# Optimization experiments

Hardware: AMD Instinct MI355X
Metric: run time of the kernel (lower is better)

## Reference

```python
import jax, jax.numpy as jnp
import numpy as np

B, L, H, D = 16, 4096, 16, 64
HID = H * D


def setup_inputs() -> dict:
    key = jax.random.key(0)
    ks = jax.random.split(key, 10)
    w = lambda k: jax.random.normal(k, (HID, HID), jnp.float32) * 0.02
    return dict(
        hidden_states=jax.random.normal(ks[0], (B, 1, HID), jnp.float32),
        past_key=jax.random.normal(ks[1], (B, H, L, D), jnp.float32),
        past_value=jax.random.normal(ks[2], (B, H, L, D), jnp.float32),
        attention_mask=jnp.ones((B, L), jnp.float32),
        cache_position=jax.random.randint(ks[3], (B, 1), 0, L, jnp.int32),
        Wq=w(ks[4]), bq=jnp.zeros((HID,), jnp.float32),
        Wk=w(ks[5]), bk=jnp.zeros((HID,), jnp.float32),
        Wv=w(ks[6]), bv=jnp.zeros((HID,), jnp.float32),
        Wo=w(ks[7]), bo=jnp.zeros((HID,), jnp.float32),
    )


def reference(hidden_states, past_key, past_value, attention_mask, cache_position,
              Wq, bq, Wk, bk, Wv, bv, Wo, bo):
    # projections: [B,1,HID]; torch Linear => x @ W.T + b
    q = hidden_states @ Wq.T + bq
    k = hidden_states @ Wk.T + bk
    v = hidden_states @ Wv.T + bv
    # [B,H,1,D]
    q = q.reshape(B, 1, H, D).transpose(0, 2, 1, 3)
    k_new = k.reshape(B, H, D)
    v_new = v.reshape(B, H, D)
    pos = cache_position[:, 0]  # [B]
    bidx = jnp.arange(B)
    # write new token K/V into cache at cache_position (per-batch)
    k_cache = past_key.at[bidx, :, pos].set(k_new)
    v_cache = past_value.at[bidx, :, pos].set(v_new)
    scale = jnp.float32(1.0) / jnp.sqrt(jnp.float32(D))
    scores = jnp.einsum('bhqd,bhkd->bhqk', q, k_cache) * scale  # [B,H,1,L]
    neg = jnp.finfo(scores.dtype).min
    scores = jnp.where(attention_mask[:, None, None, :] > 0, scores, neg)
    p = jax.nn.softmax(scores, axis=-1)
    ctx = jnp.einsum('bhqk,bhkd->bhqd', p, v_cache)  # [B,H,1,D]
    attn_output = ctx.transpose(0, 2, 1, 3).reshape(B, 1, HID) @ Wo.T + bo
    return attn_output, k_cache, v_cache
```

## Files before the change

kernel.cpp:

```cpp
#include <hip/hip_runtime.h>
#include <hip/hip_bf16.h>

#define BATCH 16
#define SEQL  4096
#define NH    16
#define HD    64
#define HID   1024
#define NCHUNK 8
#define CHUNK  (SEQL / NCHUNK)
#define KV_ELEMS (BATCH * NH * SEQL * HD)
#define PSTRIDE 68
#define C2 0.1803368801f

typedef float f4 __attribute__((ext_vector_type(4)));

__global__ __launch_bounds__(256) void gemv3(
    const float* __restrict__ x,
    const float* __restrict__ W0, const float* __restrict__ W1,
    const float* __restrict__ W2,
    const float* __restrict__ b0, const float* __restrict__ b1,
    const float* __restrict__ b2,
    float* __restrict__ out)
{
    __shared__ float xs[BATCH * HID];
    const int t = threadIdx.x;
    {
        const f4* src = (const f4*)x;
        f4* dst = (f4*)xs;
        #pragma unroll
        for (int i = 0; i < (BATCH * HID / 4) / 256; ++i)
            dst[t + i * 256] = src[t + i * 256];
    }
    __syncthreads();

    const int which = blockIdx.x >> 8;
    const int ob    = (blockIdx.x & 255) << 2;
    const float* W    = (which == 0) ? W0 : ((which == 1) ? W1 : W2);
    const float* bias = (which == 0) ? b0 : ((which == 1) ? b1 : b2);
    const int col = t >> 6, lane = t & 63;
    const int o = ob + col;
    const float* wrow = W + (size_t)o * HID;

    float acc[BATCH];
    #pragma unroll
    for (int b = 0; b < BATCH; ++b) acc[b] = 0.f;

    #pragma unroll
    for (int i = 0; i < 4; ++i) {
        const int k = (lane << 2) + (i << 8);
        const f4 w4 = *(const f4*)&wrow[k];
        #pragma unroll
        for (int b = 0; b < BATCH; ++b) {
            const f4 h4 = *(const f4*)&xs[b * HID + k];
            acc[b] += w4.x * h4.x + w4.y * h4.y + w4.z * h4.z + w4.w * h4.w;
        }
    }

    #pragma unroll
    for (int b = 0; b < BATCH; ++b) {
        #pragma unroll
        for (int sh = 1; sh < 64; sh <<= 1)
            acc[b] += __shfl_xor(acc[b], sh);
    }
    if (lane == 0) {
        const float bb = bias[o];
        #pragma unroll
        for (int b = 0; b < BATCH; ++b)
            out[which * (BATCH * HID) + b * HID + o] = acc[b] + bb;
    }
}

__global__ __launch_bounds__(256, 6) void attn_fused(
    const float* __restrict__ qkv,
    const float* __restrict__ past_k,
    const float* __restrict__ past_v,
    const float* __restrict__ mask,
    float* __restrict__ kout,
    float* __restrict__ vout,
    float* __restrict__ part)
{
    const int bh = blockIdx.x;
    const int c  = blockIdx.y;
    const int b  = bh >> 4;
    const int h  = bh & 15;
    const int t  = threadIdx.x;
    const int g  = t >> 4;
    const int j  = t & 15;

    const f4 q4 = *(const f4*)&qkv[b * HID + h * HD + (j << 2)];

    const size_t base = (size_t)bh * (SEQL * HD);
    const float* __restrict__ pkb = past_k + base;
    const float* __restrict__ pvb = past_v + base;
    float* __restrict__ kob = kout + base;
    float* __restrict__ vob = vout + base;
    const float* __restrict__ mrow = mask + b * SEQL;

    float l = 0.f;
    f4 a4 = {0.f, 0.f, 0.f, 0.f};

    #pragma unroll 1
    for (int s = 0; s < CHUNK / 128; ++s) {
        const int r0 = c * CHUNK + s * 128 + g;
        const int o0 = r0 * HD + (j << 2);

        f4 kx[8];
        float am[8];
        #pragma unroll
        for (int u = 0; u < 8; ++u)
            kx[u] = __builtin_nontemporal_load((const f4*)(pkb + o0 + u * (16 * HD)));
        #pragma unroll
        for (int u = 0; u < 8; ++u)
            am[u] = mrow[r0 + u * 16];
        #pragma unroll
        for (int u = 0; u < 8; ++u)
            __builtin_nontemporal_store(kx[u], (f4*)(kob + o0 + u * (16 * HD)));

        float p[8];
        #pragma unroll
        for (int u = 0; u < 8; ++u) {
            float d = kx[u].x * q4.x + kx[u].y * q4.y
                    + kx[u].z * q4.z + kx[u].w * q4.w;
            d += __shfl_xor(d, 1);
            d += __shfl_xor(d, 2);
            d += __shfl_xor(d, 4);
            d += __shfl_xor(d, 8);
            float pe = exp2f(d * C2);
            p[u] = (am[u] > 0.f) ? pe : 0.f;
            l += p[u];
        }

        f4 vx[8];
        #pragma unroll
        for (int u = 0; u < 8; ++u)
            vx[u] = __builtin_nontemporal_load((const f4*)(pvb + o0 + u * (16 * HD)));
        #pragma unroll
        for (int u = 0; u < 8; ++u)
            __builtin_nontemporal_store(vx[u], (f4*)(vob + o0 + u * (16 * HD)));
        #pragma unroll
        for (int u = 0; u < 8; ++u) {
            a4.x += p[u] * vx[u].x;
            a4.y += p[u] * vx[u].y;
            a4.z += p[u] * vx[u].z;
            a4.w += p[u] * vx[u].w;
        }
    }

    __shared__ float sl_[16];
    __shared__ float sa[16][64];
    if (j == 0) sl_[g] = l;
    *(f4*)&sa[g][(j << 2)] = a4;
    __syncthreads();

    float* pr = part + ((size_t)bh * NCHUNK + c) * PSTRIDE;
    if (t < 64) {
        float A = 0.f;
        #pragma unroll
        for (int gg = 0; gg < 16; ++gg) A += sa[gg][t];
        pr[1 + t] = A;
    } else if (t == 64) {
        float L = 0.f;
        #pragma unroll
        for (int gg = 0; gg < 16; ++gg) L += sl_[gg];
        pr[0] = L;
    }
}

__global__ __launch_bounds__(64) void merge_fix(
    const float* __restrict__ qkv,
    const float* __restrict__ past_k,
    const float* __restrict__ past_v,
    const float* __restrict__ mask,
    const int*   __restrict__ cpos,
    float* __restrict__ kout,
    float* __restrict__ vout,
    const float* __restrict__ part,
    float* __restrict__ ctx)
{
    const int bh = blockIdx.x;
    const int b = bh >> 4, h = bh & 15;
    const int t = threadIdx.x;
    const int pos = cpos[b];

    const size_t rowoff = (size_t)bh * (SEQL * HD) + (size_t)pos * HD + t;
    const int qo = b * HID + h * HD + t;
    const float qd  = qkv[qo];
    const float knd = qkv[BATCH * HID + qo];
    const float vnd = qkv[2 * BATCH * HID + qo];
    const float ksd = past_k[rowoff];
    const float vsd = past_v[rowoff];

    kout[rowoff] = knd;
    vout[rowoff] = vnd;

    float dst = qd * ksd, dnw = qd * knd;
    #pragma unroll
    for (int sh = 1; sh < 64; sh <<= 1) {
        dst += __shfl_xor(dst, sh);
        dnw += __shfl_xor(dnw, sh);
    }
    const float am = mask[b * SEQL + pos];
    float ps = 0.f, pn = 0.f;
    if (am > 0.f) { ps = exp2f(dst * C2); pn = exp2f(dnw * C2); }

    const int cc0 = pos / CHUNK;
    float L = 0.f, A = 0.f;
    #pragma unroll
    for (int cc = 0; cc < NCHUNK; ++cc) {
        const float* pr = part + ((size_t)bh * NCHUNK + cc) * PSTRIDE;
        float Lc = pr[0];
        float Ac = pr[1 + t];
        if (cc == cc0) { Lc += pn - ps; Ac += pn * vnd - ps * vsd; }
        L += Lc;
        A += Ac;
    }
    ctx[bh * HD + t] = A / L;
}

extern "C" void kernel_launch(void* const* d_in, const int* in_sizes, int n_in,
                              void* d_out, int out_size, void* d_ws, size_t ws_size,
                              hipStream_t stream) {
    const float* hs   = (const float*)d_in[0];
    const float* pk   = (const float*)d_in[1];
    const float* pv   = (const float*)d_in[2];
    const float* mask = (const float*)d_in[3];
    const int*   cpos = (const int*)d_in[4];
    const float* Wq   = (const float*)d_in[5];
    const float* bq   = (const float*)d_in[6];
    const float* Wk   = (const float*)d_in[7];
    const float* bk   = (const float*)d_in[8];
    const float* Wv   = (const float*)d_in[9];
    const float* bv   = (const float*)d_in[10];
    const float* Wo   = (const float*)d_in[11];
    const float* bo   = (const float*)d_in[12];

    float* out_attn = (float*)d_out;
    float* kout = out_attn + BATCH * HID;
    float* vout = kout + KV_ELEMS;

    float* ws    = (float*)d_ws;
    float* qkv   = ws;
    float* ctx   = ws + 49152;
    float* apart = ws + 65536;

    gemv3<<<dim3(768), 256, 0, stream>>>(hs, Wq, Wk, Wv, bq, bk, bv, qkv);

    attn_fused<<<dim3(256, NCHUNK), 256, 0, stream>>>(qkv, pk, pv, mask,
                                                      kout, vout, apart);
    merge_fix<<<dim3(256), 64, 0, stream>>>(qkv, pk, pv, mask, cpos,
                                            kout, vout, apart, ctx);

    gemv3<<<dim3(256), 256, 0, stream>>>(ctx, Wo, Wo, Wo, bo, bo, bo, out_attn);
}
```

Measured before the change: 219.6 us.

## Split fused attention into separate K-score and V-accumulate kernels

Replaces the single fused attention kernel with two kernels: one copies K, computes the masked exponentiated scores and writes them to a workspace along with partial denominators, and a second copies V and accumulates the weighted sum using those stored scores. The intent is to decouple the K and V streams so each kernel has a simpler memory access pattern and lower register pressure. The K/V loads also switch from nontemporal to ordinary loads. In exchange it adds an extra launch and a round trip of scores through global memory, and it takes the split path only when the workspace is large enough.

```diff
diff --git a/kernel.cpp b/kernel.cpp
--- a/kernel.cpp
+++ b/kernel.cpp
@@ -70,6 +70,125 @@
     }
 }
 
+__global__ __launch_bounds__(256, 6) void kcopy_score(
+    const float* __restrict__ qkv,
+    const float* __restrict__ past_k,
+    const float* __restrict__ mask,
+    float* __restrict__ kout,
+    float* __restrict__ pws,
+    float* __restrict__ part)
+{
+    const int bh = blockIdx.x, c = blockIdx.y;
+    const int b = bh >> 4, h = bh & 15;
+    const int t = threadIdx.x;
+    const int g = t >> 4, j = t & 15;
+
+    const f4 q4 = *(const f4*)&qkv[b * HID + h * HD + (j << 2)];
+    const size_t base = (size_t)bh * (SEQL * HD);
+    const float* __restrict__ pkb = past_k + base;
+    float* __restrict__ kob = kout + base;
+    const float* __restrict__ mrow = mask + b * SEQL;
+    float* __restrict__ prow = pws + bh * SEQL;
+
+    float l = 0.f;
+
+    #pragma unroll 1
+    for (int s = 0; s < CHUNK / 128; ++s) {
+        const int r0 = c * CHUNK + s * 128 + g;
+        const int o0 = r0 * HD + (j << 2);
+
+        f4 kx[8];
+        float am[8];
+        #pragma unroll
+        for (int u = 0; u < 8; ++u)
+            kx[u] = *(const f4*)(pkb + o0 + u * (16 * HD));
+        #pragma unroll
+        for (int u = 0; u < 8; ++u)
+            am[u] = mrow[r0 + u * 16];
+        #pragma unroll
+        for (int u = 0; u < 8; ++u)
+            __builtin_nontemporal_store(kx[u], (f4*)(kob + o0 + u * (16 * HD)));
+
+        #pragma unroll
+        for (int u = 0; u < 8; ++u) {
+            float d = kx[u].x * q4.x + kx[u].y * q4.y
+                    + kx[u].z * q4.z + kx[u].w * q4.w;
+            d += __shfl_xor(d, 1);
+            d += __shfl_xor(d, 2);
+            d += __shfl_xor(d, 4);
+            d += __shfl_xor(d, 8);
+            float pe = exp2f(d * C2);
+            const float p = (am[u] > 0.f) ? pe : 0.f;
+            l += p;
+            if (j == 0) prow[r0 + u * 16] = p;
+        }
+    }
+
+    __shared__ float sl_[16];
+    if (j == 0) sl_[g] = l;
+    __syncthreads();
+    if (t == 0) {
+        float L = 0.f;
+        #pragma unroll
+        for (int gg = 0; gg < 16; ++gg) L += sl_[gg];
+        part[((size_t)bh * NCHUNK + c) * PSTRIDE] = L;
+    }
+}
+
+__global__ __launch_bounds__(256, 6) void vcopy_acc(
+    const float* __restrict__ past_v,
+    float* __restrict__ vout,
+    const float* __restrict__ pws,
+    float* __restrict__ part)
+{
+    const int bh = blockIdx.x, c = blockIdx.y;
+    const int t = threadIdx.x;
+    const int g = t >> 4, j = t & 15;
+
+    const size_t base = (size_t)bh * (SEQL * HD);
+    const float* __restrict__ pvb = past_v + base;
+    float* __restrict__ vob = vout + base;
+    const float* __restrict__ prow = pws + bh * SEQL;
+
+    f4 a4 = {0.f, 0.f, 0.f, 0.f};
+
+    #pragma unroll 1
+    for (int s = 0; s < CHUNK / 128; ++s) {
+        const int r0 = c * CHUNK + s * 128 + g;
+        const int o0 = r0 * HD + (j << 2);
+
+        f4 vx[8];
+        float p[8];
+        #pragma unroll
+        for (int u = 0; u < 8; ++u)
+            vx[u] = *(const f4*)(pvb + o0 + u * (16 * HD));
+        #pragma unroll
+        for (int u = 0; u < 8; ++u)
+            p[u] = prow[r0 + u * 16];
+        #pragma unroll
+        for (int u = 0; u < 8; ++u)
+            __builtin_nontemporal_store(vx[u], (f4*)(vob + o0 + u * (16 * HD)));
+        #pragma unroll
+        for (int u = 0; u < 8; ++u) {
+            a4.x += p[u] * vx[u].x;
+            a4.y += p[u] * vx[u].y;
+            a4.z += p[u] * vx[u].z;
+            a4.w += p[u] * vx[u].w;
+        }
+    }
+
+    __shared__ float sa[16][64];
+    *(f4*)&sa[g][(j << 2)] = a4;
+    __syncthreads();
+
+    if (t < 64) {
+        float A = 0.f;
+        #pragma unroll
+        for (int gg = 0; gg < 16; ++gg) A += sa[gg][t];
+        part[((size_t)bh * NCHUNK + c) * PSTRIDE + 1 + t] = A;
+    }
+}
+
 __global__ __launch_bounds__(256, 6) void attn_fused(
     const float* __restrict__ qkv,
     const float* __restrict__ past_k,
@@ -79,16 +198,12 @@
     float* __restrict__ vout,
     float* __restrict__ part)
 {
-    const int bh = blockIdx.x;
-    const int c  = blockIdx.y;
-    const int b  = bh >> 4;
-    const int h  = bh & 15;
-    const int t  = threadIdx.x;
-    const int g  = t >> 4;
-    const int j  = t & 15;
+    const int bh = blockIdx.x, c = blockIdx.y;
+    const int b = bh >> 4, h = bh & 15;
+    const int t = threadIdx.x;
+    const int g = t >> 4, j = t & 15;
 
     const f4 q4 = *(const f4*)&qkv[b * HID + h * HD + (j << 2)];
-
     const size_t base = (size_t)bh * (SEQL * HD);
     const float* __restrict__ pkb = past_k + base;
     const float* __restrict__ pvb = past_v + base;
@@ -242,11 +357,21 @@
     float* qkv   = ws;
     float* ctx   = ws + 49152;
     float* apart = ws + 65536;
+    float* pws   = ws + 204800;
+
+    const bool split_ok = ws_size >= (size_t)1253376 * sizeof(float);
 
     gemv3<<<dim3(768), 256, 0, stream>>>(hs, Wq, Wk, Wv, bq, bk, bv, qkv);
 
-    attn_fused<<<dim3(256, NCHUNK), 256, 0, stream>>>(qkv, pk, pv, mask,
-                                                      kout, vout, apart);
+    if (split_ok) {
+        kcopy_score<<<dim3(256, NCHUNK), 256, 0, stream>>>(qkv, pk, mask,
+                                                           kout, pws, apart);
+        vcopy_acc<<<dim3(256, NCHUNK), 256, 0, stream>>>(pv, vout, pws, apart);
+    } else {
+        attn_fused<<<dim3(256, NCHUNK), 256, 0, stream>>>(qkv, pk, pv, mask,
+                                                          kout, vout, apart);
+    }
+
     merge_fix<<<dim3(256), 64, 0, stream>>>(qkv, pk, pv, mask, cpos,
                                             kout, vout, apart, ctx);
 
```

After: 229.9 us. +4.7%, slower.

## Replace chunked attention with grid-strided tile sweep and per-tile partials

Applied to the files above, without the earlier changes.

Adds a new attention kernel that splits the KV cache into 65536 tiles of 16 rows and sweeps them with 2048 persistent blocks in a grid-stride loop. Each iteration prefetches the next tile's K/V while copying and reducing the current one, and writes per-tile partial sums to workspace. A new merge kernel then reduces the 256 partials per head. The aim is more parallelism and software prefetching to keep HBM busy, at the cost of two block barriers per tile, more partial-sum traffic, and a dependence on the workspace being large enough (otherwise the old path runs).

```diff
diff --git a/kernel.cpp b/kernel.cpp
--- a/kernel.cpp
+++ b/kernel.cpp
@@ -6,11 +6,16 @@
 #define NH    16
 #define HD    64
 #define HID   1024
+#define KV_ELEMS (BATCH * NH * SEQL * HD)
+#define C2 0.1803368801f
+
+#define NBLK  2048
+#define NTILE 65536
+#define TPB   (NTILE / NBLK)
+
 #define NCHUNK 8
-#define CHUNK  (SEQL / NCHUNK)
-#define KV_ELEMS (BATCH * NH * SEQL * HD)
+#define CHUNK  512
 #define PSTRIDE 68
-#define C2 0.1803368801f
 
 typedef float f4 __attribute__((ext_vector_type(4)));
 
@@ -68,6 +73,133 @@
         for (int b = 0; b < BATCH; ++b)
             out[which * (BATCH * HID) + b * HID + o] = acc[b] + bb;
     }
+}
+
+__global__ __launch_bounds__(256, 8) void attn_sweep(
+    const float* __restrict__ qkv,
+    const float* __restrict__ past_k,
+    const float* __restrict__ past_v,
+    const float* __restrict__ mask,
+    float* __restrict__ kout,
+    float* __restrict__ vout,
+    float* __restrict__ Aws,
+    float* __restrict__ Lws)
+{
+    const int blk = blockIdx.x;
+    const int t   = threadIdx.x;
+    const int g   = t >> 4;
+    const int j   = t & 15;
+    const int w   = t >> 6;
+
+    __shared__ float sw[4][64];
+    __shared__ float slw[4];
+
+    int tile = blk;
+    size_t off = (size_t)tile * 1024 + (t << 2);
+    f4 k0 = __builtin_nontemporal_load((const f4*)(past_k + off));
+    f4 v0 = __builtin_nontemporal_load((const f4*)(past_v + off));
+    f4 q0 = *(const f4*)&qkv[(tile >> 8) * HD + (j << 2)];
+    float am0 = mask[((tile >> 12) << 12) + ((tile & 255) << 4) + g];
+
+    #pragma unroll 1
+    for (int tau = 0; tau < TPB; ++tau) {
+        const size_t coff = off;
+        const int ctile = tile;
+        const f4 kc = k0, vc = v0, qc = q0;
+        const float amc = am0;
+
+        if (tau < TPB - 1) {
+            tile += NBLK;
+            off = (size_t)tile * 1024 + (t << 2);
+            k0 = __builtin_nontemporal_load((const f4*)(past_k + off));
+            v0 = __builtin_nontemporal_load((const f4*)(past_v + off));
+            q0 = *(const f4*)&qkv[(tile >> 8) * HD + (j << 2)];
+            am0 = mask[((tile >> 12) << 12) + ((tile & 255) << 4) + g];
+        }
+
+        __builtin_nontemporal_store(kc, (f4*)(kout + coff));
+        __builtin_nontemporal_store(vc, (f4*)(vout + coff));
+
+        float d = kc.x * qc.x + kc.y * qc.y + kc.z * qc.z + kc.w * qc.w;
+        d += __shfl_xor(d, 1);
+        d += __shfl_xor(d, 2);
+        d += __shfl_xor(d, 4);
+        d += __shfl_xor(d, 8);
+        float pe = exp2f(d * C2);
+        const float p = (amc > 0.f) ? pe : 0.f;
+
+        f4 c4 = { p * vc.x, p * vc.y, p * vc.z, p * vc.w };
+        float pw = p;
+        c4.x += __shfl_xor(c4.x, 16);  c4.x += __shfl_xor(c4.x, 32);
+        c4.y += __shfl_xor(c4.y, 16);  c4.y += __shfl_xor(c4.y, 32);
+        c4.z += __shfl_xor(c4.z, 16);  c4.z += __shfl_xor(c4.z, 32);
+        c4.w += __shfl_xor(c4.w, 16);  c4.w += __shfl_xor(c4.w, 32);
+        pw  += __shfl_xor(pw, 16);     pw  += __shfl_xor(pw, 32);
+
+        if (((t >> 4) & 3) == 0) *(f4*)&sw[w][j << 2] = c4;
+        if ((t & 63) == 0) slw[w] = pw;
+        __syncthreads();
+
+        if (t < 64) {
+            const float A = sw[0][t] + sw[1][t] + sw[2][t] + sw[3][t];
+            Aws[((size_t)ctile << 6) + t] = A;
+            if (t == 0)
+                Lws[ctile] = slw[0] + slw[1] + slw[2] + slw[3];
+        }
+        __syncthreads();
+    }
+}
+
+__global__ __launch_bounds__(64) void merge2(
+    const float* __restrict__ qkv,
+    const float* __restrict__ past_k,
+    const float* __restrict__ past_v,
+    const float* __restrict__ mask,
+    const int*   __restrict__ cpos,
+    float* __restrict__ kout,
+    float* __restrict__ vout,
+    const float* __restrict__ Aws,
+    const float* __restrict__ Lws,
+    float* __restrict__ ctx)
+{
+    const int bh = blockIdx.x;
+    const int b = bh >> 4;
+    const int t = threadIdx.x;
+    const int pos = cpos[b];
+
+    float L = 0.f, A = 0.f;
+    const float* Ab = Aws + ((size_t)bh << 14);
+    const float* Lb = Lws + bh * 256;
+    #pragma unroll 4
+    for (int i = 0; i < 256; ++i) {
+        A += Ab[(i << 6) + t];
+        L += Lb[i];
+    }
+
+    const size_t rowoff = (size_t)bh * (SEQL * HD) + (size_t)pos * HD + t;
+    const int qo = bh * HD + t;
+    const float qd  = qkv[qo];
+    const float knd = qkv[BATCH * HID + qo];
+    const float vnd = qkv[2 * BATCH * HID + qo];
+    const float ksd = past_k[rowoff];
+    const float vsd = past_v[rowoff];
+
+    kout[rowoff] = knd;
+    vout[rowoff] = vnd;
+
+    float dst = qd * ksd, dnw = qd * knd;
+    #pragma unroll
+    for (int sh = 1; sh < 64; sh <<= 1) {
+        dst += __shfl_xor(dst, sh);
+        dnw += __shfl_xor(dnw, sh);
+    }
+    const float am = mask[b * SEQL + pos];
+    float ps = 0.f, pn = 0.f;
+    if (am > 0.f) { ps = exp2f(dst * C2); pn = exp2f(dnw * C2); }
+
+    L += pn - ps;
+    A += pn * vnd - ps * vsd;
+    ctx[bh * HD + t] = A / L;
 }
 
 __global__ __launch_bounds__(256, 6) void attn_fused(
@@ -79,16 +211,12 @@
     float* __restrict__ vout,
     float* __restrict__ part)
 {
-    const int bh = blockIdx.x;
-    const int c  = blockIdx.y;
-    const int b  = bh >> 4;
-    const int h  = bh & 15;
-    const int t  = threadIdx.x;
-    const int g  = t >> 4;
-    const int j  = t & 15;
+    const int bh = blockIdx.x, c = blockIdx.y;
+    const int b = bh >> 4, h = bh & 15;
+    const int t = threadIdx.x;
+    const int g = t >> 4, j = t & 15;
 
     const f4 q4 = *(const f4*)&qkv[b * HID + h * HD + (j << 2)];
-
     const size_t base = (size_t)bh * (SEQL * HD);
     const float* __restrict__ pkb = past_k + base;
     const float* __restrict__ pvb = past_v + base;
@@ -178,12 +306,12 @@
     float* __restrict__ ctx)
 {
     const int bh = blockIdx.x;
-    const int b = bh >> 4, h = bh & 15;
+    const int b = bh >> 4;
     const int t = threadIdx.x;
     const int pos = cpos[b];
 
     const size_t rowoff = (size_t)bh * (SEQL * HD) + (size_t)pos * HD + t;
-    const int qo = b * HID + h * HD + t;
+    const int qo = bh * HD + t;
     const float qd  = qkv[qo];
     const float knd = qkv[BATCH * HID + qo];
     const float vnd = qkv[2 * BATCH * HID + qo];
@@ -242,13 +370,25 @@
     float* qkv   = ws;
     float* ctx   = ws + 49152;
     float* apart = ws + 65536;
+    float* Lws   = ws + 65536;
+    float* Aws   = ws + 131072;
+
+    const size_t need_sweep = (size_t)(131072 + (size_t)NTILE * 64) * sizeof(float);
+    const bool sweep_ok = ws_size >= need_sweep;
 
     gemv3<<<dim3(768), 256, 0, stream>>>(hs, Wq, Wk, Wv, bq, bk, bv, qkv);
 
-    attn_fused<<<dim3(256, NCHUNK), 256, 0, stream>>>(qkv, pk, pv, mask,
-                                                      kout, vout, apart);
-    merge_fix<<<dim3(256), 64, 0, stream>>>(qkv, pk, pv, mask, cpos,
-                                            kout, vout, apart, ctx);
+    if (sweep_ok) {
+        attn_sweep<<<dim3(NBLK), 256, 0, stream>>>(qkv, pk, pv, mask,
+                                                   kout, vout, Aws, Lws);
+        merge2<<<dim3(256), 64, 0, stream>>>(qkv, pk, pv, mask, cpos,
+                                             kout, vout, Aws, Lws, ctx);
+    } else {
+        attn_fused<<<dim3(256, NCHUNK), 256, 0, stream>>>(qkv, pk, pv, mask,
+                                                          kout, vout, apart);
+        merge_fix<<<dim3(256), 64, 0, stream>>>(qkv, pk, pv, mask, cpos,
+                                                kout, vout, apart, ctx);
+    }
 
     gemv3<<<dim3(256), 256, 0, stream>>>(ctx, Wo, Wo, Wo, bo, bo, bo, out_attn);
 }
```

Measured after the change: 241.0 us. 9.7% more time.
